# Kernel optimization log

Hardware: AMD Instinct MI355X
Metric: run time of the kernel (lower is better)

## Reference

```python
import jax, jax.numpy as jnp
import numpy as np

EPS_LOG = 1e-10
DECAY = 0.99
RESET_THRESHOLD = 2


def setup_inputs() -> dict:
    key = jax.random.key(0)
    ks = jax.random.split(key, 8)
    B, C_in, T = 4, 1024, 2048
    K, D = 8192, 256
    N = B * T
    return {
        "z": jax.random.normal(ks[0], (B, C_in, T), dtype=jnp.float32),
        "u": jax.random.uniform(ks[1], (N, K), dtype=jnp.float32),
        "Wi": jax.random.normal(ks[2], (D, C_in), dtype=jnp.float32) * 0.02,
        "bi": jax.random.normal(ks[3], (D,), dtype=jnp.float32) * 0.02,
        "Wo": jax.random.normal(ks[4], (C_in, D), dtype=jnp.float32) * 0.02,
        "bo": jax.random.normal(ks[5], (C_in,), dtype=jnp.float32) * 0.02,
        "embedding": jax.random.normal(ks[6], (K, D), dtype=jnp.float32),
        "cluster_size": jnp.zeros((K,), dtype=jnp.float32),
    }


def reference(z, u, Wi, bi, Wo, bo, embedding, cluster_size):
    B, _, T = z.shape
    K, D = embedding.shape
    N = B * T

    # inproj: Conv1d with kernel_size=1 == pointwise linear over channel dim
    z_e = jnp.einsum('bit,di->bdt', z, Wi) + bi[None, :, None]  # (B, D, T)
    z_d = z_e.transpose(0, 2, 1).reshape(N, D)                   # (b t) d

    # squared-euclidean distances via norm expansion
    dist = ((z_d ** 2).sum(axis=1, keepdims=True)
            - 2.0 * (z_d @ embedding.T)
            + (embedding ** 2).sum(axis=1))                      # (N, K)

    # gumbel noise (training=True), softmax_temp = 1.0
    gumbel = -jnp.log(-jnp.log(u + EPS_LOG) + EPS_LOG)
    logits = -dist + gumbel
    y_soft = jax.nn.softmax(logits, axis=-1)                     # (N, K)

    z_q_flat = y_soft @ embedding                                # (N, D)

    # kl_div(log(avg+eps), uniform target of shape (N,K), reduction='sum')
    avg_probs = y_soft.mean(axis=0)                              # (K,)
    inv_k = 1.0 / K
    kl_loss = N * jnp.sum(inv_k * (jnp.log(inv_k) - jnp.log(avg_probs + EPS_LOG)))

    indices = jnp.argmax(y_soft, axis=1)                         # (N,) int

    z_q = z_q_flat.reshape(B, T, D).transpose(0, 2, 1)           # (B, D, T)
    vq_loss = jnp.mean((z_e - jax.lax.stop_gradient(z_q)) ** 2)

    # outproj: Conv1d kernel_size=1
    out = jnp.einsum('bdt,od->bot', z_q, Wo) + bo[None, :, None]  # (B, C_in, T)

    # box_result: active_num uses cluster_size BEFORE the EMA update
    active_num = (cluster_size > RESET_THRESHOLD).sum().astype(z.dtype)
    counts = jnp.zeros((K,), z.dtype).at[indices].add(1.0)       # one-hot column sums
    probs = counts / N                                           # == mean(one_hot, axis=0)
    perplexity = jnp.exp(-jnp.sum(probs * jnp.log(probs + EPS_LOG)))
    new_cluster_size = cluster_size * DECAY + counts * (1.0 - DECAY)

    return out, vq_loss, kl_loss, perplexity, active_num, new_cluster_size
```

## Files before the change

### kernel.cpp

```cpp
#include <hip/hip_runtime.h>
#include <hip/hip_fp16.h>


#define NROWS 8192
#define KCL   8192
#define DDIM  256
#define CIN   1024
#define TSEQ  2048
#define EPSL  1e-10f
#define MHAT  (-140.0f)

#define OUT_SC   (4*CIN*TSEQ)

#define ZD_OFF   0
#define ZQ_OFF   (NROWS*DDIM)
#define E2_OFF   (2*NROWS*DDIM)
#define CS_OFF   (E2_OFF + KCL)
#define CNT_OFF  (CS_OFF + KCL)
#define VQ_OFF   (CNT_OFF + KCL)
#define LINV_OFF (VQ_OFF + 4)

#define ZD2W   0
#define ZQ2W   2097152
#define EBW    4194304
#define ETW    5242880
#define WOBW   6291456
#define ZFW    6422528
#define E2W    7471104
#define C2W    7479296
#define LINVW  7487488
#define CSUMW  7495680
#define CNTW   7503872
#define VQW    7512064
#define PW     7512128
#define ENDW   (PW + 33554432)

using short8v = __attribute__((ext_vector_type(8))) short;
using short4v = __attribute__((ext_vector_type(4))) short;
using f32x16  = __attribute__((ext_vector_type(16))) float;

__device__ __forceinline__ ushort f2bf(float f) {
  unsigned int x = __float_as_uint(f);
  return (ushort)((x + 0x7FFFu + ((x >> 16) & 1u)) >> 16);
}
__device__ __forceinline__ float bf2f(ushort h) {
  return __uint_as_float(((unsigned int)h) << 16);
}
__device__ __forceinline__ short8v pack8(float4 a, float4 b) {
  short8v v;
  v[0] = (short)f2bf(a.x); v[1] = (short)f2bf(a.y);
  v[2] = (short)f2bf(a.z); v[3] = (short)f2bf(a.w);
  v[4] = (short)f2bf(b.x); v[5] = (short)f2bf(b.y);
  v[6] = (short)f2bf(b.z); v[7] = (short)f2bf(b.w);
  return v;
}
__device__ __forceinline__ void gload16(const void* g, void* l) {
  __builtin_amdgcn_global_load_lds(
      (const __attribute__((address_space(1))) unsigned int*)g,
      (__attribute__((address_space(3))) unsigned int*)l, 16, 0, 0);
}


__global__ __launch_bounds__(256) void e2_kernel(const float* __restrict__ E,
                                                 float* __restrict__ e2) {
  const int tid = threadIdx.x;
  const int k = blockIdx.x * 64 + (tid >> 2);
  const int p = tid & 3;
  const float* row = E + (size_t)k * DDIM + p * 64;
  float s = 0.f;
#pragma unroll
  for (int j = 0; j < 16; ++j) {
    const float4 v = *reinterpret_cast<const float4*>(row + j * 4);
    s += v.x * v.x + v.y * v.y + v.z * v.z + v.w * v.w;
  }
  s += __shfl_xor(s, 1);
  s += __shfl_xor(s, 2);
  if (p == 0) e2[k] = s;
}

__global__ __launch_bounds__(256) void e2c2_kernel(const float* __restrict__ E,
                                                   float* __restrict__ e2,
                                                   float* __restrict__ c2) {
  const int tid = threadIdx.x;
  const int k = blockIdx.x * 64 + (tid >> 2);
  const int p = tid & 3;
  const float* row = E + (size_t)k * DDIM + p * 64;
  float s = 0.f;
#pragma unroll
  for (int j = 0; j < 16; ++j) {
    const float4 v = *reinterpret_cast<const float4*>(row + j * 4);
    s += v.x * v.x + v.y * v.y + v.z * v.z + v.w * v.w;
  }
  s += __shfl_xor(s, 1);
  s += __shfl_xor(s, 2);
  if (p == 0) { e2[k] = s; c2[k] = -s - MHAT; }
}

__global__ __launch_bounds__(256) void cvtwob_kernel(const float* __restrict__ W,
                                                     ushort* __restrict__ Wb) {
  const size_t i = ((size_t)blockIdx.x * 256 + threadIdx.x) * 8;
  const float4 a = *reinterpret_cast<const float4*>(W + i);
  const float4 b = *reinterpret_cast<const float4*>(W + i + 4);
  *reinterpret_cast<short8v*>(Wb + i) = pack8(a, b);
}

__global__ __launch_bounds__(256) void etprep_kernel(const float* __restrict__ E,
                                                     ushort* __restrict__ ET,
                                                     ushort* __restrict__ EB) {
  __shared__ float tb[64 * 68];
  const int t = threadIdx.x;
  const int kb = (blockIdx.x & 127) * 64;
  const int db = (blockIdx.x >> 7) * 64;
#pragma unroll
  for (int it = 0; it < 4; ++it) {
    const int r = (t >> 4) + it * 16;
    const int c = (t & 15) * 4;
    const float4 v = *reinterpret_cast<const float4*>(E + (size_t)(kb + r) * DDIM + db + c);
    tb[r * 68 + c] = v.x; tb[r * 68 + c + 1] = v.y;
    tb[r * 68 + c + 2] = v.z; tb[r * 68 + c + 3] = v.w;
    short4v o;
    o[0] = (short)f2bf(v.x); o[1] = (short)f2bf(v.y);
    o[2] = (short)f2bf(v.z); o[3] = (short)f2bf(v.w);
    *reinterpret_cast<short4v*>(EB + (size_t)(kb + r) * DDIM + db + c) = o;
  }
  __syncthreads();
  const int dl = t >> 2, kg = (t & 3) * 16;
  short8v o0, o1;
#pragma unroll
  for (int j = 0; j < 8; ++j) o0[j] = (short)f2bf(tb[(kg + j) * 68 + dl]);
#pragma unroll
  for (int j = 0; j < 8; ++j) o1[j] = (short)f2bf(tb[(kg + 8 + j) * 68 + dl]);
  ushort* dst = ET + (size_t)(db + dl) * KCL + kb + kg;
  *reinterpret_cast<short8v*>(dst) = o0;
  *reinterpret_cast<short8v*>(dst + 8) = o1;
}

__global__ __launch_bounds__(256) void cvtzf_kernel(const float* __restrict__ zd,
                                                    ushort* __restrict__ zf) {
  const int t = threadIdx.x;
  const int g = blockIdx.x;
  const int lane = t & 63, row = lane & 31, half = lane >> 5;
  const float* zr = zd + (size_t)(g * 32 + row) * DDIM + half * 8;
  ushort* dst = zf + ((size_t)g * 16 * 64 + lane) * 8;
#pragma unroll
  for (int i = 0; i < 4; ++i) {
    const int ks = (t >> 6) * 4 + i;
    const float4 a = *reinterpret_cast<const float4*>(zr + ks * 16);
    const float4 b = *reinterpret_cast<const float4*>(zr + ks * 16 + 4);
    *reinterpret_cast<short8v*>(dst + (size_t)ks * 64 * 8) = pack8(a, b);
  }
}

__global__ __launch_bounds__(256) void inproj32_kernel(const float* __restrict__ z,
                                                       const float* __restrict__ Wi,
                                                       const float* __restrict__ bi,
                                                       float* __restrict__ zd) {
  __shared__ float wi_s[32 * 260];
  __shared__ float zc[32 * 32];
  const int tid = threadIdx.x;
  const int nb = blockIdx.x >> 1, cih = blockIdx.x & 1;
  const int n0 = nb * 32;
  const int b = n0 / TSEQ;
  const int t0 = n0 % TSEQ;
  const float* zb = z + (size_t)b * CIN * TSEQ;
  const int ibase = cih * 512;

  const int dg = tid & 63;
  const int d0 = dg * 4;
  const int wv = tid >> 6;
  const int r0 = wv * 8;

  float acc[4][8];
#pragma unroll
  for (int c = 0; c < 4; ++c)
#pragma unroll
    for (int r = 0; r < 8; ++r) acc[c][r] = 0.f;

  for (int i0 = ibase; i0 < ibase + 512; i0 += 32) {
    __syncthreads();
    {
      const int iiq = (tid & 7) * 4;
      const int dt = tid >> 3;
#pragma unroll
      for (int p = 0; p < 8; ++p) {
        const int d = dt + p * 32;
        const float4 w = *reinterpret_cast<const float4*>(Wi + (size_t)d * CIN + i0 + iiq);
        wi_s[(iiq + 0) * 260 + d] = w.x;
        wi_s[(iiq + 1) * 260 + d] = w.y;
        wi_s[(iiq + 2) * 260 + d] = w.z;
        wi_s[(iiq + 3) * 260 + d] = w.w;
      }
      const int rr = tid & 31;
      const int iib = tid >> 5;
#pragma unroll
      for (int p = 0; p < 4; ++p) {
        const int ii = iib + p * 8;
        zc[ii * 32 + rr] = zb[(size_t)(i0 + ii) * TSEQ + t0 + rr];
      }
    }
    __syncthreads();
#pragma unroll
    for (int ii = 0; ii < 32; ++ii) {
      const float4 w = *reinterpret_cast<const float4*>(&wi_s[ii * 260 + d0]);
#pragma unroll
      for (int rq = 0; rq < 2; ++rq) {
        const float4 zv = *reinterpret_cast<const float4*>(&zc[ii * 32 + r0 + rq * 4]);
        const float zz[4] = {zv.x, zv.y, zv.z, zv.w};
#pragma unroll
        for (int q = 0; q < 4; ++q) {
          acc[0][rq * 4 + q] += w.x * zz[q];
          acc[1][rq * 4 + q] += w.y * zz[q];
          acc[2][rq * 4 + q] += w.z * zz[q];
          acc[3][rq * 4 + q] += w.w * zz[q];
        }
      }
    }
  }
  const float4 bv = *reinterpret_cast<const float4*>(bi + d0);
  const float bx = cih ? 0.f : bv.x, by = cih ? 0.f : bv.y;
  const float bz = cih ? 0.f : bv.z, bw = cih ? 0.f : bv.w;
#pragma unroll
  for (int r = 0; r < 8; ++r) {
    float* zr = zd + (size_t)(n0 + r0 + r) * DDIM + d0;
    atomicAdd(zr + 0, acc[0][r] + bx);
    atomicAdd(zr + 1, acc[1][r] + by);
    atomicAdd(zr + 2, acc[2][r] + bz);
    atomicAdd(zr + 3, acc[3][r] + bw);
  }
}

#define FSTEP(KT, CUR, UC, UN)                                                 \
  {                                                                            \
    const int k0 = kbase + (KT) * 32;                                          \
    __syncthreads();            \
    if ((KT) < 15) {                                                           \
      _Pragma("unroll")                                                        \
      for (int pp = 0; pp < 2; ++pp) {                                         \
        const int q = tid + pp * 512, r = q >> 5, c = q & 31;                  \
        gload16(Eb + (size_t)(k0 + 32 + r) * 256 + (size_t)(c ^ (r & 7)) * 8,  \
                &Es[(1 - (CUR)) * 8192 + q * 8]);                              \
      }                                                                        \
      const float* ubn = ubase + k0 + 32 + r31;                                \
      _Pragma("unroll")                                                        \
      for (int reg = 0; reg < 16; ++reg) {                                     \
        const int dr = (reg & 3) + 8 * (reg >> 2);                             \
        UN[reg] = ubn[(size_t)dr << 13];                                       \
      }                                                                        \
    }                                                                          \
    const float ce = c2[k0 + r31];                                             \
    const ushort* Ecur = Es + (CUR) * 8192;                                    \
    f32x16 acc;                                                                \
    _Pragma("unroll")                                                          \
    for (int i = 0; i < 16; ++i) acc[i] = 0.f;                                 \
    _Pragma("unroll")                                                          \
    for (int ks = 0; ks < 16; ++ks) {                                          \
      const int cc = (ks * 2 + half) ^ (r31 & 7);                              \
      const short8v B =                                                        \
          *reinterpret_cast<const short8v*>(Ecur + r31 * 256 + cc * 8);        \
      acc = __builtin_amdgcn_mfma_f32_32x32x16_bf16(A[ks], B, acc, 0, 0, 0);   \
    }                                                                          \
    ushort* pdst = P + (size_t)rowu * KCL + k0 + r31;                          \
    _Pragma("unroll")                                                          \
    for (int reg = 0; reg < 16; ++reg) {                                       \
      const int dr = (reg & 3) + 8 * (reg >> 2);                               \
      const float D = 1e-10f - __logf(UC[reg] + 1e-10f);                       \
      const float pe = __fdividef(__expf(fmaf(acc[reg], 2.f, ce)), D);         \
      pdst[(size_t)dr << 13] = f2bf(pe);                                       \
    }                                                                          \
  }

__global__ __launch_bounds__(512, 2) void flash4_kernel(
    const ushort* __restrict__ ZF, const float* __restrict__ u,
    const ushort* __restrict__ Eb, const float* __restrict__ c2,
    ushort* __restrict__ P) {
  __shared__ ushort Es[2 * 32 * 256];
  const int tid = threadIdx.x;
  const int l = tid & 63, w = tid >> 6;
  const int half = l >> 5;
  const int swz = (blockIdx.x & 7) * 64 + (blockIdx.x >> 3);
  const int nb = swz & 31, kq = swz >> 5;
  const int n0 = nb * 256;
  const int kbase = kq * 512;
  const int r31 = l & 31;

  short8v A[16];
  {
    const ushort* zf = ZF + ((size_t)(nb * 8 + w) * 16 * 64 + l) * 8;
#pragma unroll
    for (int ks = 0; ks < 16; ++ks)
      A[ks] = *reinterpret_cast<const short8v*>(zf + (size_t)ks * 512);
  }

  const int rowu = n0 + w * 32 + 4 * half;
  const float* ubase = u + ((size_t)rowu << 13);

#pragma unroll
  for (int pp = 0; pp < 2; ++pp) {
    const int q = tid + pp * 512, r = q >> 5, c = q & 31;
    gload16(Eb + (size_t)(kbase + r) * 256 + (size_t)(c ^ (r & 7)) * 8, &Es[q * 8]);
  }
  float uA[16], uB[16];
  {
    const float* ub = ubase + kbase + r31;
#pragma unroll
    for (int reg = 0; reg < 16; ++reg) {
      const int dr = (reg & 3) + 8 * (reg >> 2);
      uA[reg] = ub[(size_t)dr << 13];
    }
  }

  for (int kt2 = 0; kt2 < 16; kt2 += 2) {
    FSTEP(kt2, 0, uA, uB);
    FSTEP(kt2 + 1, 1, uB, uA);
  }
}

__global__ __launch_bounds__(256) void rowpass_kernel(
    const ushort* __restrict__ P, const float* __restrict__ zd,
    const float* __restrict__ E, const float* __restrict__ e2,
    const float* __restrict__ u, float* __restrict__ linv,
    float* __restrict__ counts) {
  const int l = threadIdx.x & 63;
  const int w = threadIdx.x >> 6;
  const int n = blockIdx.x * 4 + w;
  const ushort* pr = P + (size_t)n * KCL;
  float lsum = 0.f;
  float bv[4] = {-1.f, -1.f, -1.f, -1.f};
  int bi[4] = {0x7fffffff, 0x7fffffff, 0x7fffffff, 0x7fffffff};
  for (int it = 0; it < 16; ++it) {
    const short8v v = *reinterpret_cast<const short8v*>(pr + it * 512 + l * 8);
#pragma unroll
    for (int j = 0; j < 8; ++j) {
      const float f = bf2f((ushort)v[j]);
      lsum += f;
      const int kk = it * 512 + l * 8 + j;
      const bool c0 = f > bv[0], c1 = f > bv[1];
      const float n1 = c0 ? bv[0] : f; const int i1 = c0 ? bi[0] : kk;
      bv[1] = c1 ? n1 : bv[1]; bi[1] = c1 ? i1 : bi[1];
      bv[0] = c0 ? f : bv[0];  bi[0] = c0 ? kk : bi[0];
    }
  }
#pragma unroll
  for (int mk = 1; mk < 64; mk <<= 1) {
    lsum += __shfl_xor(lsum, mk);
    float ov[4]; int oi[4];
#pragma unroll
    for (int i = 0; i < 4; ++i) { ov[i] = __shfl_xor(bv[i], mk); oi[i] = __shfl_xor(bi[i], mk); }
#pragma unroll
    for (int i = 0; i < 4; ++i) {
      const float f = ov[i]; const int kk = oi[i];
      const bool c0 = (f > bv[0]) || (f == bv[0] && kk < bi[0]);
      const bool c1 = (f > bv[1]) || (f == bv[1] && kk < bi[1]);
      const bool c2 = (f > bv[2]) || (f == bv[2] && kk < bi[2]);
      const bool c3 = (f > bv[3]) || (f == bv[3] && kk < bi[3]);
      const float n3 = c2 ? bv[2] : f; const int i3 = c2 ? bi[2] : kk;
      const float n2 = c1 ? bv[1] : f; const int i2 = c1 ? bi[1] : kk;
      const float n1 = c0 ? bv[0] : f; const int i1 = c0 ? bi[0] : kk;
      bv[3] = c3 ? n3 : bv[3]; bi[3] = c3 ? i3 : bi[3];
      bv[2] = c2 ? n2 : bv[2]; bi[2] = c2 ? i2 : bi[2];
      bv[1] = c1 ? n1 : bv[1]; bi[1] = c1 ? i1 : bi[1];
      bv[0] = c0 ? f : bv[0];  bi[0] = c0 ? kk : bi[0];
    }
  }
  const float4 zv = *reinterpret_cast<const float4*>(zd + (size_t)n * DDIM + l * 4);
  float best = -1e30f; int besti = 0x7fffffff;
#pragma unroll
  for (int c = 0; c < 4; ++c) {
    const int kc = bi[c];
    const float4 ev = *reinterpret_cast<const float4*>(E + (size_t)kc * DDIM + l * 4);
    float d = zv.x * ev.x + zv.y * ev.y + zv.z * ev.z + zv.w * ev.w;
#pragma unroll
    for (int mk = 1; mk < 64; mk <<= 1) d += __shfl_xor(d, mk);
    const float uu = u[(size_t)n * KCL + kc];
    const float D = 1e-10f - __logf(uu + 1e-10f);
    const float g = -__logf(D);
    const float lg = 2.f * d - e2[kc] + g;
    if (lg > best || (lg == best && kc < besti)) { best = lg; besti = kc; }
  }
  if (l == 0) {
    atomicAdd(&counts[besti], 1.f);
    linv[n] = 1.f / lsum;
  }
}

__global__ __launch_bounds__(512, 2) void pv2_kernel(
    const ushort* __restrict__ P, const ushort* __restrict__ ET,
    const float* __restrict__ linv, float* __restrict__ parts,
    float* __restrict__ colsum) {
  __shared__ ushort ps[64 * 64];
  __shared__ ushort es[256 * 64];
  __shared__ float linv_s[64];
  const int tid = threadIdx.x;
  const int l = tid & 63, w = tid >> 6;
  const int half = l >> 5;
  const int r31 = l & 31;
  const int swz = (blockIdx.x & 7) * 64 + (blockIdx.x >> 3);
  const int nb = swz & 127, ks = swz >> 7;
  const int n0 = nb * 64;
  const int kc0 = ks * 2048;
  const int nw = w & 1, dw = w >> 1;

  if (tid < 64) linv_s[tid] = linv[n0 + tid];

  f32x16 acc0, acc1;
#pragma unroll
  for (int i = 0; i < 16; ++i) { acc0[i] = 0.f; acc1[i] = 0.f; }

  short8v rp, re[4];
  {
    const int r = tid >> 3, c = tid & 7;
    rp = *reinterpret_cast<const short8v*>(P + (size_t)(n0 + r) * KCL + kc0 + c * 8);
#pragma unroll
    for (int pp = 0; pp < 4; ++pp) {
      const int q = tid * 4 + pp; const int rr = q >> 3, cc = q & 7;
      re[pp] = *reinterpret_cast<const short8v*>(ET + (size_t)rr * KCL + kc0 + cc * 8);
    }
  }
  for (int t = 0; t < 32; ++t) {
    {
      const int r = tid >> 3, c = tid & 7;
      *reinterpret_cast<short8v*>(ps + r * 64 + ((c ^ (r & 7))) * 8) = rp;
    }
#pragma unroll
    for (int pp = 0; pp < 4; ++pp) {
      const int q = tid * 4 + pp; const int rr = q >> 3, cc = q & 7;
      *reinterpret_cast<short8v*>(es + rr * 64 + ((cc ^ (rr & 7))) * 8) = re[pp];
    }
    __syncthreads();
    if (t < 31) {
      const int kc = kc0 + (t + 1) * 64;
      {
        const int r = tid >> 3, c = tid & 7;
        rp = *reinterpret_cast<const short8v*>(P + (size_t)(n0 + r) * KCL + kc + c * 8);
      }
#pragma unroll
      for (int pp = 0; pp < 4; ++pp) {
        const int q = tid * 4 + pp; const int rr = q >> 3, cc = q & 7;
        re[pp] = *reinterpret_cast<const short8v*>(ET + (size_t)rr * KCL + kc + cc * 8);
      }
    }
#pragma unroll
    for (int ksn = 0; ksn < 4; ++ksn) {
      const int cc = ksn * 2 + half;
      short8v a, b0, b1;
      { const int r = nw * 32 + r31;      a  = *reinterpret_cast<const short8v*>(ps + r * 64 + ((cc ^ (r & 7))) * 8); }
      { const int r = dw * 64 + r31;      b0 = *reinterpret_cast<const short8v*>(es + r * 64 + ((cc ^ (r & 7))) * 8); }
      { const int r = dw * 64 + 32 + r31; b1 = *reinterpret_cast<const short8v*>(es + r * 64 + ((cc ^ (r & 7))) * 8); }
      acc0 = __builtin_amdgcn_mfma_f32_32x32x16_bf16(a, b0, acc0, 0, 0, 0);
      acc1 = __builtin_amdgcn_mfma_f32_32x32x16_bf16(a, b1, acc1, 0, 0, 0);
    }
    {
      const int c = tid >> 3;
      const int rb = tid & 7;
      float csp = 0.f;
#pragma unroll
      for (int r8 = 0; r8 < 8; ++r8) {
        const int r = rb + r8 * 8;
        const int chunk = (c >> 3) ^ (r & 7);
        csp += bf2f(ps[r * 64 + chunk * 8 + (c & 7)]) * linv_s[r];
      }
      csp += __shfl_xor(csp, 1);
      csp += __shfl_xor(csp, 2);
      csp += __shfl_xor(csp, 4);
      if (rb == 0) atomicAdd(&colsum[kc0 + t * 64 + c], csp);
    }
    __syncthreads();
  }
  float* pbase = parts + (size_t)ks * NROWS * DDIM;
#pragma unroll
  for (int reg = 0; reg < 16; ++reg) {
    const int dr = (reg & 3) + 8 * (reg >> 2) + 4 * half;
    float* zr = pbase + (size_t)(n0 + nw * 32 + dr) * DDIM + dw * 64 + r31;
    zr[0]  = acc0[reg];
    zr[32] = acc1[reg];
  }
}

__global__ __launch_bounds__(256) void zqred_kernel(const float* __restrict__ parts,
                                                    const float* __restrict__ linv,
                                                    const float* __restrict__ zd,
                                                    float* __restrict__ zq,
                                                    float* __restrict__ vqs) {
  const size_t i = ((size_t)blockIdx.x * 256 + threadIdx.x) * 8;
  const int n = (int)(i >> 8);
  const float lv = linv[n];
  float s = 0.f;
#pragma unroll
  for (int j = 0; j < 8; j += 4) {
    float4 p0 = *reinterpret_cast<const float4*>(parts + i + j);
    const float4 p1 = *reinterpret_cast<const float4*>(parts + i + j + (size_t)NROWS * DDIM);
    const float4 p2 = *reinterpret_cast<const float4*>(parts + i + j + (size_t)2 * NROWS * DDIM);
    const float4 p3 = *reinterpret_cast<const float4*>(parts + i + j + (size_t)3 * NROWS * DDIM);
    const float4 a = *reinterpret_cast<const float4*>(zd + i + j);
    float4 o;
    o.x = (p0.x + p1.x + p2.x + p3.x) * lv;
    o.y = (p0.y + p1.y + p2.y + p3.y) * lv;
    o.z = (p0.z + p1.z + p2.z + p3.z) * lv;
    o.w = (p0.w + p1.w + p2.w + p3.w) * lv;
    *reinterpret_cast<float4*>(zq + i + j) = o;
    const float dx = a.x - o.x, dy = a.y - o.y, dz = a.z - o.z, dw = a.w - o.w;
    s += dx * dx + dy * dy + dz * dz + dw * dw;
  }
#pragma unroll
  for (int mk = 1; mk < 64; mk <<= 1) s += __shfl_xor(s, mk);
  if ((threadIdx.x & 63) == 0) atomicAdd(vqs, s);
}

__global__ __launch_bounds__(256) void outproj2_kernel(const float* __restrict__ zq,
                                                       const ushort* __restrict__ Wob,
                                                       const float* __restrict__ bo,
                                                       float* __restrict__ outp) {
  extern __shared__ char smem[];
  ushort* zs = (ushort*)smem;
  ushort* wsld = zs + 64 * 256;
  const int tid = threadIdx.x;
  const int l = tid & 63, w = tid >> 6;
  const int half = l >> 5;
  const int nb = blockIdx.x >> 4, ob = blockIdx.x & 15;
  const int n0 = nb * 64, o0 = ob * 64;
  const int nw = w & 1, ow = w >> 1;
  {
    const int row = tid >> 2, seg = tid & 3;
    const float* zr = zq + (size_t)(n0 + row) * DDIM + seg * 64;
    const ushort* wr = Wob + (size_t)(o0 + row) * DDIM + seg * 64;
#pragma unroll
    for (int g = 0; g < 8; ++g) {
      const float4 a = *reinterpret_cast<const float4*>(zr + g * 8);
      const float4 b = *reinterpret_cast<const float4*>(zr + g * 8 + 4);
      const int c = seg * 8 + g;
      *reinterpret_cast<short8v*>(zs + row * 256 + ((c ^ (row & 7))) * 8) = pack8(a, b);
      const short8v wv = *reinterpret_cast<const short8v*>(wr + g * 8);
      *reinterpret_cast<short8v*>(wsld + row * 256 + ((c ^ (row & 7))) * 8) = wv;
    }
  }
  __syncthreads();
  f32x16 acc;
#pragma unroll
  for (int i = 0; i < 16; ++i) acc[i] = 0.f;
#pragma unroll
  for (int ksn = 0; ksn < 16; ++ksn) {
    const int cc = ksn * 2 + half;
    const int ra = nw * 32 + (l & 31);
    const int rb = ow * 32 + (l & 31);
    const short8v a = *reinterpret_cast<const short8v*>(zs + ra * 256 + ((cc ^ (ra & 7))) * 8);
    const short8v b = *reinterpret_cast<const short8v*>(wsld + rb * 256 + ((cc ^ (rb & 7))) * 8);
    acc = __builtin_amdgcn_mfma_f32_32x32x16_bf16(a, b, acc, 0, 0, 0);
  }
  const int o = o0 + ow * 32 + (l & 31);
  const float bvv = bo[o];
  const int nbase = n0 + nw * 32 + 4 * half;
#pragma unroll
  for (int rq = 0; rq < 4; ++rq) {
    const int n = nbase + rq * 8;
    const int b = n >> 11;
    const int tt = n & 2047;
    float4 ov;
    ov.x = acc[rq * 4 + 0] + bvv;
    ov.y = acc[rq * 4 + 1] + bvv;
    ov.z = acc[rq * 4 + 2] + bvv;
    ov.w = acc[rq * 4 + 3] + bvv;
    *reinterpret_cast<float4*>(outp + ((size_t)b * CIN + o) * TSEQ + tt) = ov;
  }
}

template <bool STORE_LG>
__global__ __launch_bounds__(512) void flash_kernel(
    const float* __restrict__ zd, const float* __restrict__ u,
    const float* __restrict__ E, const float* __restrict__ e2g,
    float* __restrict__ zq, float* __restrict__ colsum,
    float* __restrict__ counts, float* __restrict__ vqsum,
    float* __restrict__ linvg, __half* __restrict__ lgbuf) {
  extern __shared__ float lds[];
  float* zs = lds;
  float* es = zs + 32 * 260;
  float* e2t = es + 64 * 260;
  float* cst = e2t + 64;
  float* red = cst + 64;

  const int tid = threadIdx.x;
  const int lane = tid & 63;
  const int wv = tid >> 6;
  const int r = (lane >> 4) & 3;
  const int kg = lane & 15;
  const int row = wv * 4 + r;
  const int n0 = blockIdx.x * 32;
  const int n = n0 + row;

  {
    const int rr = tid >> 4;
    const int iq = tid & 15;
#pragma unroll
    for (int p = 0; p < 4; ++p) {
      const int i = iq * 16 + p * 4;
      *reinterpret_cast<float4*>(&zs[rr * 260 + i]) =
          *reinterpret_cast<const float4*>(zd + (size_t)(n0 + rr) * DDIM + i);
    }
  }

  float4 accp[4];
#pragma unroll
  for (int s = 0; s < 4; ++s) accp[s] = make_float4(0.f, 0.f, 0.f, 0.f);
  float lsum = 0.f;
  float best = -1e30f;
  int bidx = 0;

  const float* zrow = zs + row * 260;

  for (int t = 0; t < KCL / 64; ++t) {
    const int k0 = t * 64;
    __syncthreads();
    {
      const int iq = tid & 15;
#pragma unroll
      for (int pp = 0; pp < 2; ++pp) {
        const int kk = (tid >> 4) + pp * 32;
#pragma unroll
        for (int p = 0; p < 4; ++p) {
          const int i = iq * 16 + p * 4;
          *reinterpret_cast<float4*>(&es[kk * 260 + i]) =
              *reinterpret_cast<const float4*>(E + (size_t)(k0 + kk) * DDIM + i);
        }
      }
      if (tid < 64) e2t[tid] = e2g[k0 + tid];
    }
    __syncthreads();

    float acc4[4] = {0.f, 0.f, 0.f, 0.f};
#pragma unroll 4
    for (int i = 0; i < DDIM; i += 4) {
      const float4 zv = *reinterpret_cast<const float4*>(zrow + i);
#pragma unroll
      for (int jj = 0; jj < 4; ++jj) {
        const float4 ev = *reinterpret_cast<const float4*>(&es[(kg + jj * 16) * 260 + i]);
        acc4[jj] += zv.x * ev.x + zv.y * ev.y + zv.z * ev.z + zv.w * ev.w;
      }
    }

    float p4[4];
    float tmax = -1e30f;
    int tidx = 0;
#pragma unroll
    for (int jj = 0; jj < 4; ++jj) {
      const int kk = kg + jj * 16;
      const float uu = u[(size_t)n * KCL + k0 + kk];
      const float g = -__logf(-__logf(uu + EPSL) + EPSL);
      const float lt = 2.f * acc4[jj] - e2t[kk] + g - MHAT;
      const float pe = __expf(lt);
      p4[jj] = pe;
      lsum += pe;
      if (lt > tmax) { tmax = lt; tidx = k0 + kk; }
    }
#pragma unroll
    for (int mk = 1; mk <= 8; mk <<= 1) {
      const float ov = __shfl_xor(tmax, mk);
      const int oi = __shfl_xor(tidx, mk);
      if (ov > tmax || (ov == tmax && oi < tidx)) { tmax = ov; tidx = oi; }
    }
    if (tmax > best) { best = tmax; bidx = tidx; }

#pragma unroll
    for (int jj = 0; jj < 4; ++jj) {
#pragma unroll 4
      for (int q = 0; q < 16; ++q) {
        const int kk = jj * 16 + q;
        const float yv = __shfl(p4[jj], (lane & 48) | q);
        const float* erow = &es[kk * 260 + kg * 16];
#pragma unroll
        for (int s = 0; s < 4; ++s) {
          const int c = (s + kg) & 3;
          const float4 ev = *reinterpret_cast<const float4*>(erow + c * 4);
          accp[s].x += yv * ev.x;
          accp[s].y += yv * ev.y;
          accp[s].z += yv * ev.z;
          accp[s].w += yv * ev.w;
        }
      }
    }
  }

#pragma unroll
  for (int mk = 1; mk <= 8; mk <<= 1) lsum += __shfl_xor(lsum, mk);
  const float linv = 1.0f / lsum;

  if (kg == 0) {
    atomicAdd(&counts[bidx], 1.0f);
    linvg[n] = linv;
  }

  float vqp = 0.f;
#pragma unroll
  for (int s = 0; s < 4; ++s) {
    const int c = (s + kg) & 3;
    const int d = kg * 16 + c * 4;
    float4 o;
    o.x = accp[s].x * linv;
    o.y = accp[s].y * linv;
    o.z = accp[s].z * linv;
    o.w = accp[s].w * linv;
    *reinterpret_cast<float4*>(zq + (size_t)n * DDIM + d) = o;
    const float4 zv = *reinterpret_cast<const float4*>(zrow + d);
    const float dx = zv.x - o.x, dy = zv.y - o.y, dz = zv.z - o.z, dw = zv.w - o.w;
    vqp += dx * dx + dy * dy + dz * dz + dw * dw;
  }
#pragma unroll
  for (int mk = 1; mk <= 32; mk <<= 1) vqp += __shfl_xor(vqp, mk);
  if (lane == 0) red[wv] = vqp;
  __syncthreads();
  if (tid == 0) {
    float s = 0.f;
#pragma unroll
    for (int ww = 0; ww < 8; ++ww) s += red[ww];
    atomicAdd(vqsum, s);
  }

  if (!STORE_LG) {
    if (tid < 64) cst[tid] = 0.f;
    for (int t = 0; t < KCL / 64; ++t) {
      const int k0 = t * 64;
      __syncthreads();
      {
        const int iq = tid & 15;
#pragma unroll
        for (int pp = 0; pp < 2; ++pp) {
          const int kk = (tid >> 4) + pp * 32;
#pragma unroll
          for (int p = 0; p < 4; ++p) {
            const int i = iq * 16 + p * 4;
            *reinterpret_cast<float4*>(&es[kk * 260 + i]) =
                *reinterpret_cast<const float4*>(E + (size_t)(k0 + kk) * DDIM + i);
          }
        }
        if (tid < 64) e2t[tid] = e2g[k0 + tid];
      }
      __syncthreads();
      float acc4[4] = {0.f, 0.f, 0.f, 0.f};
#pragma unroll 4
      for (int i = 0; i < DDIM; i += 4) {
        const float4 zv = *reinterpret_cast<const float4*>(zrow + i);
#pragma unroll
        for (int jj = 0; jj < 4; ++jj) {
          const float4 ev = *reinterpret_cast<const float4*>(&es[(kg + jj * 16) * 260 + i]);
          acc4[jj] += zv.x * ev.x + zv.y * ev.y + zv.z * ev.z + zv.w * ev.w;
        }
      }
      float cs4[4];
#pragma unroll
      for (int jj = 0; jj < 4; ++jj) {
        const int kk = kg + jj * 16;
        const float uu = u[(size_t)n * KCL + k0 + kk];
        const float g = -__logf(-__logf(uu + EPSL) + EPSL);
        const float lt = 2.f * acc4[jj] - e2t[kk] + g - MHAT;
        cs4[jj] = __expf(lt) * linv;
      }
#pragma unroll
      for (int mk = 16; mk <= 32; mk <<= 1)
#pragma unroll
        for (int jj = 0; jj < 4; ++jj) cs4[jj] += __shfl_xor(cs4[jj], mk);
      if (lane < 16) {
#pragma unroll
        for (int jj = 0; jj < 4; ++jj) atomicAdd(&cst[kg + jj * 16], cs4[jj]);
      }
      __syncthreads();
      if (tid < 64) {
        atomicAdd(&colsum[k0 + tid], cst[tid]);
        cst[tid] = 0.f;
      }
    }
  }
}

__global__ __launch_bounds__(256) void outproj_kernel(const float* __restrict__ zq,
                                                      const float* __restrict__ Wo,
                                                      const float* __restrict__ bo,
                                                      float* __restrict__ outp) {
  __shared__ float wo_s[32 * 260];
  __shared__ float zc[32 * 68];
  const int tid = threadIdx.x;
  const int n0 = (blockIdx.x >> 2) * 64;
  const int ot = (blockIdx.x & 3) * 256;
  const int b = n0 / TSEQ;
  const int t0 = n0 % TSEQ;

  const int og = tid & 63;
  const int o0 = og * 4;
  const int wv = tid >> 6;
  const int r0 = wv * 16;

  float acc[4][16];
#pragma unroll
  for (int c = 0; c < 4; ++c)
#pragma unroll
    for (int r = 0; r < 16; ++r) acc[c][r] = 0.f;

  for (int dd = 0; dd < DDIM; dd += 32) {
    __syncthreads();
    {
      const int ccq = (tid & 7) * 4;
      const int oq = tid >> 3;
#pragma unroll
      for (int p = 0; p < 8; ++p) {
        const int oo = oq + p * 32;
        const float4 w = *reinterpret_cast<const float4*>(Wo + (size_t)(ot + oo) * DDIM + dd + ccq);
        wo_s[(ccq + 0) * 260 + oo] = w.x;
        wo_s[(ccq + 1) * 260 + oo] = w.y;
        wo_s[(ccq + 2) * 260 + oo] = w.z;
        wo_s[(ccq + 3) * 260 + oo] = w.w;
      }
#pragma unroll
      for (int p = 0; p < 2; ++p) {
        const int rr = oq + p * 32;
        const float4 v = *reinterpret_cast<const float4*>(zq + (size_t)(n0 + rr) * DDIM + dd + ccq);
        zc[(ccq + 0) * 68 + rr] = v.x;
        zc[(ccq + 1) * 68 + rr] = v.y;
        zc[(ccq + 2) * 68 + rr] = v.z;
        zc[(ccq + 3) * 68 + rr] = v.w;
      }
    }
    __syncthreads();
#pragma unroll
    for (int cc = 0; cc < 32; ++cc) {
      const float4 w = *reinterpret_cast<const float4*>(&wo_s[cc * 260 + o0]);
#pragma unroll
      for (int rq = 0; rq < 4; ++rq) {
        const float4 zv = *reinterpret_cast<const float4*>(&zc[cc * 68 + r0 + rq * 4]);
        const float zz[4] = {zv.x, zv.y, zv.z, zv.w};
#pragma unroll
        for (int q = 0; q < 4; ++q) {
          acc[0][rq * 4 + q] += w.x * zz[q];
          acc[1][rq * 4 + q] += w.y * zz[q];
          acc[2][rq * 4 + q] += w.z * zz[q];
          acc[3][rq * 4 + q] += w.w * zz[q];
        }
      }
    }
  }
  const float4 bv = *reinterpret_cast<const float4*>(bo + ot + o0);
  float* ob = outp + (size_t)b * CIN * TSEQ + t0;
  const float bb[4] = {bv.x, bv.y, bv.z, bv.w};
#pragma unroll
  for (int c = 0; c < 4; ++c) {
#pragma unroll
    for (int rq = 0; rq < 4; ++rq) {
      float4 o;
      o.x = acc[c][rq * 4 + 0] + bb[c];
      o.y = acc[c][rq * 4 + 1] + bb[c];
      o.z = acc[c][rq * 4 + 2] + bb[c];
      o.w = acc[c][rq * 4 + 3] + bb[c];
      *reinterpret_cast<float4*>(ob + (size_t)(ot + o0 + c) * TSEQ + r0 + rq * 4) = o;
    }
  }
}

__global__ __launch_bounds__(256) void finalize_kernel(
    const float* __restrict__ colsum, const float* __restrict__ counts,
    const float* __restrict__ vqsum, const float* __restrict__ csin,
    float* __restrict__ outsc, float* __restrict__ ncs) {
  __shared__ float rS[3][4];
  const int tid = threadIdx.x;
  const int lane = tid & 63;
  const int wv = tid >> 6;
  float sLog = 0.f, sH = 0.f, sAct = 0.f;
  for (int k = tid; k < KCL; k += 256) {
    const float avg = colsum[k] * (1.0f / NROWS);
    sLog += __logf(avg + EPSL);
    const float pb = counts[k] * (1.0f / NROWS);
    sH += pb * __logf(pb + EPSL);
    sAct += (csin[k] > 2.0f) ? 1.f : 0.f;
    ncs[k] = csin[k] * 0.99f + counts[k] * 0.01f;
  }
#pragma unroll
  for (int mk = 1; mk <= 32; mk <<= 1) {
    sLog += __shfl_xor(sLog, mk);
    sH += __shfl_xor(sH, mk);
    sAct += __shfl_xor(sAct, mk);
  }
  if (lane == 0) { rS[0][wv] = sLog; rS[1][wv] = sH; rS[2][wv] = sAct; }
  __syncthreads();
  if (tid == 0) {
    float SL = 0.f, SH = 0.f, SA = 0.f;
#pragma unroll
    for (int w = 0; w < 4; ++w) { SL += rS[0][w]; SH += rS[1][w]; SA += rS[2][w]; }
    outsc[0] = vqsum[0] * (1.0f / ((float)NROWS * (float)DDIM));
    outsc[1] = (float)NROWS * __logf(1.0f / (float)KCL) - SL;
    outsc[2] = __expf(-SH);
    outsc[3] = SA;
  }
}

extern "C" void kernel_launch(void* const* d_in, const int* in_sizes, int n_in,
                              void* d_out, int out_size, void* d_ws, size_t ws_size,
                              hipStream_t stream) {
  (void)in_sizes; (void)n_in; (void)out_size;
  const float* z = (const float*)d_in[0];
  const float* u = (const float*)d_in[1];
  const float* Wi = (const float*)d_in[2];
  const float* bi = (const float*)d_in[3];
  const float* Wo = (const float*)d_in[4];
  const float* bo = (const float*)d_in[5];
  const float* E = (const float*)d_in[6];
  const float* csin = (const float*)d_in[7];
  float* outp = (float*)d_out;
  float* ws = (float*)d_ws;

  const size_t needNew = (size_t)ENDW * 4;
  if (ws_size >= needNew) {
    ushort* EB = (ushort*)(ws + EBW);
    ushort* ET = (ushort*)(ws + ETW);
    ushort* WOB = (ushort*)(ws + WOBW);
    ushort* ZF = (ushort*)(ws + ZFW);
    ushort* P = (ushort*)(ws + PW);

    hipMemsetAsync((void*)(ws + CSUMW), 0, (size_t)(2 * KCL + 64) * 4, stream);
    hipMemsetAsync((void*)(ws + ZD2W), 0, (size_t)NROWS * DDIM * 4, stream);

    e2c2_kernel<<<KCL / 64, 256, 0, stream>>>(E, ws + E2W, ws + C2W);
    etprep_kernel<<<512, 256, 0, stream>>>(E, ET, EB);
    cvtwob_kernel<<<128, 256, 0, stream>>>(Wo, WOB);
    inproj32_kernel<<<512, 256, 0, stream>>>(z, Wi, bi, ws + ZD2W);
    cvtzf_kernel<<<NROWS / 32, 256, 0, stream>>>(ws + ZD2W, ZF);

    flash4_kernel<<<512, 512, 0, stream>>>(ZF, u, EB, ws + C2W, P);
    rowpass_kernel<<<NROWS / 4, 256, 0, stream>>>(P, ws + ZD2W, E, ws + E2W, u,
                                                  ws + LINVW, ws + CNTW);
    pv2_kernel<<<512, 512, 0, stream>>>(P, ET, ws + LINVW, outp, ws + CSUMW);
    zqred_kernel<<<1024, 256, 0, stream>>>(outp, ws + LINVW, ws + ZD2W,
                                           ws + ZQ2W, ws + VQW);

    hipFuncSetAttribute(reinterpret_cast<const void*>(&outproj2_kernel),
                        hipFuncAttributeMaxDynamicSharedMemorySize, 65536);
    outproj2_kernel<<<2048, 256, 65536, stream>>>(ws + ZQ2W, WOB, bo, outp);
    finalize_kernel<<<1, 256, 0, stream>>>(ws + CSUMW, ws + CNTW, ws + VQW,
                                           csin, outp + OUT_SC, outp + OUT_SC + 4);
  } else {
    hipMemsetAsync((void*)(ws + CS_OFF), 0, (size_t)(2 * KCL + 1) * sizeof(float), stream);
    hipMemsetAsync((void*)(ws + ZD_OFF), 0, (size_t)NROWS * DDIM * 4, stream);
    e2_kernel<<<KCL / 64, 256, 0, stream>>>(E, ws + E2_OFF);
    inproj32_kernel<<<512, 256, 0, stream>>>(z, Wi, bi, ws + ZD_OFF);
    const int ldsB = (32 * 260 + 64 * 260 + 64 + 64 + 16) * 4;
    hipFuncSetAttribute(reinterpret_cast<const void*>(&flash_kernel<false>),
                        hipFuncAttributeMaxDynamicSharedMemorySize, ldsB);
    flash_kernel<false><<<NROWS / 32, 512, ldsB, stream>>>(
        ws + ZD_OFF, u, E, ws + E2_OFF, ws + ZQ_OFF, ws + CS_OFF, ws + CNT_OFF,
        ws + VQ_OFF, ws + LINV_OFF, (__half*)nullptr);
    outproj_kernel<<<(NROWS / 64) * 4, 256, 0, stream>>>(ws + ZQ_OFF, Wo, bo, outp);
    finalize_kernel<<<1, 256, 0, stream>>>(ws + CS_OFF, ws + CNT_OFF, ws + VQ_OFF,
                                           csin, outp + OUT_SC, outp + OUT_SC + 4);
  }
}
```

Before: 512.0 us.

## Fuse row sums and top-2 argmax into flash kernel, drop P re-read pass

```diff
diff --git a/kernel.cpp b/kernel.cpp
--- a/kernel.cpp
+++ b/kernel.cpp
@@ -25,7 +25,7 @@
 #define EBW    4194304
 #define ETW    5242880
 #define WOBW   6291456
-#define ZFW    6422528
+#define ZDBW   6422528
 #define E2W    7471104
 #define C2W    7479296
 #define LINVW  7487488
@@ -34,6 +34,9 @@
 #define VQW    7512064
 #define PW     7512128
 #define ENDW   (PW + 33554432)
+#define LSPW   ZQ2W
+#define CVW    (ZQ2W + 131072)
+#define CIW    (ZQ2W + 393216)
 
 using short8v = __attribute__((ext_vector_type(8))) short;
 using short4v = __attribute__((ext_vector_type(4))) short;
@@ -133,22 +136,6 @@
   ushort* dst = ET + (size_t)(db + dl) * KCL + kb + kg;
   *reinterpret_cast<short8v*>(dst) = o0;
   *reinterpret_cast<short8v*>(dst + 8) = o1;
-}
-
-__global__ __launch_bounds__(256) void cvtzf_kernel(const float* __restrict__ zd,
-                                                    ushort* __restrict__ zf) {
-  const int t = threadIdx.x;
-  const int g = blockIdx.x;
-  const int lane = t & 63, row = lane & 31, half = lane >> 5;
-  const float* zr = zd + (size_t)(g * 32 + row) * DDIM + half * 8;
-  ushort* dst = zf + ((size_t)g * 16 * 64 + lane) * 8;
-#pragma unroll
-  for (int i = 0; i < 4; ++i) {
-    const int ks = (t >> 6) * 4 + i;
-    const float4 a = *reinterpret_cast<const float4*>(zr + ks * 16);
-    const float4 b = *reinterpret_cast<const float4*>(zr + ks * 16 + 4);
-    *reinterpret_cast<short8v*>(dst + (size_t)ks * 64 * 8) = pack8(a, b);
-  }
 }
 
 __global__ __launch_bounds__(256) void inproj32_kernel(const float* __restrict__ z,
@@ -229,7 +216,7 @@
   }
 }
 
-#define FSTEP(KT, CUR, UC, UN)                                                 \
+#define FSS(KT, CUR, UC, UN)                                                   \
   {                                                                            \
     const int k0 = kbase + (KT) * 32;                                          \
     __syncthreads();            \
@@ -240,14 +227,11 @@
         gload16(Eb + (size_t)(k0 + 32 + r) * 256 + (size_t)(c ^ (r & 7)) * 8,  \
                 &Es[(1 - (CUR)) * 8192 + q * 8]);                              \
       }                                                                        \
-      const float* ubn = ubase + k0 + 32 + r31;                                \
+      const float* ubn = ubase + k0 + 32 + 4 * half;                           \
       _Pragma("unroll")                                                        \
-      for (int reg = 0; reg < 16; ++reg) {                                     \
-        const int dr = (reg & 3) + 8 * (reg >> 2);                             \
-        UN[reg] = ubn[(size_t)dr << 13];                                       \
-      }                                                                        \
+      for (int q = 0; q < 4; ++q)                                              \
+        UN[q] = *reinterpret_cast<const float4*>(ubn + q * 8);                 \
     }                                                                          \
-    const float ce = c2[k0 + r31];                                             \
     const ushort* Ecur = Es + (CUR) * 8192;                                    \
     f32x16 acc;                                                                \
     _Pragma("unroll")                                                          \
@@ -255,25 +239,40 @@
     _Pragma("unroll")                                                          \
     for (int ks = 0; ks < 16; ++ks) {                                          \
       const int cc = (ks * 2 + half) ^ (r31 & 7);                              \
-      const short8v B =                                                        \
+      const short8v Af =                                                       \
           *reinterpret_cast<const short8v*>(Ecur + r31 * 256 + cc * 8);        \
-      acc = __builtin_amdgcn_mfma_f32_32x32x16_bf16(A[ks], B, acc, 0, 0, 0);   \
+      acc = __builtin_amdgcn_mfma_f32_32x32x16_bf16(Af, ZB[ks], acc, 0, 0, 0); \
     }                                                                          \
-    ushort* pdst = P + (size_t)rowu * KCL + k0 + r31;                          \
+    ushort* pdst = P + (size_t)n * KCL + k0 + 4 * half;                        \
     _Pragma("unroll")                                                          \
-    for (int reg = 0; reg < 16; ++reg) {                                       \
-      const int dr = (reg & 3) + 8 * (reg >> 2);                               \
-      const float D = 1e-10f - __logf(UC[reg] + 1e-10f);                       \
-      const float pe = __fdividef(__expf(fmaf(acc[reg], 2.f, ce)), D);         \
-      pdst[(size_t)dr << 13] = f2bf(pe);                                       \
+    for (int q = 0; q < 4; ++q) {                                              \
+      const float uu[4] = {UC[q].x, UC[q].y, UC[q].z, UC[q].w};                \
+      short4v st;                                                              \
+      _Pragma("unroll")                                                        \
+      for (int j = 0; j < 4; ++j) {                                            \
+        const int reg = q * 4 + j;                                             \
+        const int kcl = k0 + q * 8 + 4 * half + j;                             \
+        const float ce = c2s[kcl - kbase];                                     \
+        const float D = 1e-10f - __logf(uu[j] + 1e-10f);                       \
+        const float pe = __fdividef(__expf(fmaf(acc[reg], 2.f, ce)), D);       \
+        psum += pe;                                                            \
+        const bool cA = pe > b0v, cB = pe > b1v;                               \
+        const float nv = cA ? b0v : pe; const int ni = cA ? b0i : kcl;         \
+        b1v = cB ? nv : b1v; b1i = cB ? ni : b1i;                              \
+        b0v = cA ? pe : b0v; b0i = cA ? kcl : b0i;                             \
+        st[j] = (short)f2bf(pe);                                               \
+      }                                                                        \
+      *reinterpret_cast<short4v*>(pdst + q * 8) = st;                          \
     }                                                                          \
   }
 
-__global__ __launch_bounds__(512, 2) void flash4_kernel(
-    const ushort* __restrict__ ZF, const float* __restrict__ u,
+__global__ __launch_bounds__(512, 2) void flashS_kernel(
+    const ushort* __restrict__ ZDB, const float* __restrict__ u,
     const ushort* __restrict__ Eb, const float* __restrict__ c2,
-    ushort* __restrict__ P) {
+    ushort* __restrict__ P, float* __restrict__ lsp,
+    float* __restrict__ candv, int* __restrict__ candi) {
   __shared__ ushort Es[2 * 32 * 256];
+  __shared__ float c2s[512];
   const int tid = threadIdx.x;
   const int l = tid & 63, w = tid >> 6;
   const int half = l >> 5;
@@ -282,67 +281,84 @@
   const int n0 = nb * 256;
   const int kbase = kq * 512;
   const int r31 = l & 31;
-
-  short8v A[16];
+  const int n = n0 + w * 32 + r31;
+
+  short8v ZB[16];
   {
-    const ushort* zf = ZF + ((size_t)(nb * 8 + w) * 16 * 64 + l) * 8;
+    const ushort* zr = ZDB + (size_t)n * DDIM + half * 8;
 #pragma unroll
     for (int ks = 0; ks < 16; ++ks)
-      A[ks] = *reinterpret_cast<const short8v*>(zf + (size_t)ks * 512);
-  }
-
-  const int rowu = n0 + w * 32 + 4 * half;
-  const float* ubase = u + ((size_t)rowu << 13);
+      ZB[ks] = *reinterpret_cast<const short8v*>(zr + ks * 16);
+  }
+
+  const float* ubase = u + ((size_t)n << 13);
+  c2s[tid] = c2[kbase + tid];
 
 #pragma unroll
   for (int pp = 0; pp < 2; ++pp) {
     const int q = tid + pp * 512, r = q >> 5, c = q & 31;
     gload16(Eb + (size_t)(kbase + r) * 256 + (size_t)(c ^ (r & 7)) * 8, &Es[q * 8]);
   }
-  float uA[16], uB[16];
+  float4 uA[4], uB[4];
   {
-    const float* ub = ubase + kbase + r31;
-#pragma unroll
-    for (int reg = 0; reg < 16; ++reg) {
-      const int dr = (reg & 3) + 8 * (reg >> 2);
-      uA[reg] = ub[(size_t)dr << 13];
-    }
-  }
+    const float* ub = ubase + kbase + 4 * half;
+#pragma unroll
+    for (int q = 0; q < 4; ++q)
+      uA[q] = *reinterpret_cast<const float4*>(ub + q * 8);
+  }
+
+  float psum = 0.f;
+  float b0v = -1.f, b1v = -1.f;
+  int b0i = 0x7fffffff, b1i = 0x7fffffff;
 
   for (int kt2 = 0; kt2 < 16; kt2 += 2) {
-    FSTEP(kt2, 0, uA, uB);
-    FSTEP(kt2 + 1, 1, uB, uA);
-  }
-}
-
-__global__ __launch_bounds__(256) void rowpass_kernel(
-    const ushort* __restrict__ P, const float* __restrict__ zd,
+    FSS(kt2, 0, uA, uB);
+    FSS(kt2 + 1, 1, uB, uA);
+  }
+
+  psum += __shfl_xor(psum, 32);
+  {
+    const float ov0 = __shfl_xor(b0v, 32); const int oi0 = __shfl_xor(b0i, 32);
+    const float ov1 = __shfl_xor(b1v, 32); const int oi1 = __shfl_xor(b1i, 32);
+    {
+      const bool cA = (ov0 > b0v) || (ov0 == b0v && oi0 < b0i);
+      const bool cB = (ov0 > b1v) || (ov0 == b1v && oi0 < b1i);
+      const float nv = cA ? b0v : ov0; const int ni = cA ? b0i : oi0;
+      b1v = cB ? nv : b1v; b1i = cB ? ni : b1i;
+      b0v = cA ? ov0 : b0v; b0i = cA ? oi0 : b0i;
+    }
+    {
+      const bool cA = (ov1 > b0v) || (ov1 == b0v && oi1 < b0i);
+      const bool cB = (ov1 > b1v) || (ov1 == b1v && oi1 < b1i);
+      const float nv = cA ? b0v : ov1; const int ni = cA ? b0i : oi1;
+      b1v = cB ? nv : b1v; b1i = cB ? ni : b1i;
+      b0v = cA ? ov1 : b0v; b0i = cA ? oi1 : b0i;
+    }
+  }
+  if (half == 0) {
+    lsp[kq * NROWS + n] = psum;
+    candv[(kq * 2 + 0) * NROWS + n] = b0v;
+    candi[(kq * 2 + 0) * NROWS + n] = b0i;
+    candv[(kq * 2 + 1) * NROWS + n] = b1v;
+    candi[(kq * 2 + 1) * NROWS + n] = b1i;
+  }
+}
+
+__global__ __launch_bounds__(256) void rowfin_kernel(
+    const float* __restrict__ lsp, const float* __restrict__ candv,
+    const int* __restrict__ candi, const float* __restrict__ zd,
     const float* __restrict__ E, const float* __restrict__ e2,
     const float* __restrict__ u, float* __restrict__ linv,
     float* __restrict__ counts) {
   const int l = threadIdx.x & 63;
   const int w = threadIdx.x >> 6;
   const int n = blockIdx.x * 4 + w;
-  const ushort* pr = P + (size_t)n * KCL;
-  float lsum = 0.f;
+
   float bv[4] = {-1.f, -1.f, -1.f, -1.f};
   int bi[4] = {0x7fffffff, 0x7fffffff, 0x7fffffff, 0x7fffffff};
-  for (int it = 0; it < 16; ++it) {
-    const short8v v = *reinterpret_cast<const short8v*>(pr + it * 512 + l * 8);
-#pragma unroll
-    for (int j = 0; j < 8; ++j) {
-      const float f = bf2f((ushort)v[j]);
-      lsum += f;
-      const int kk = it * 512 + l * 8 + j;
-      const bool c0 = f > bv[0], c1 = f > bv[1];
-      const float n1 = c0 ? bv[0] : f; const int i1 = c0 ? bi[0] : kk;
-      bv[1] = c1 ? n1 : bv[1]; bi[1] = c1 ? i1 : bi[1];
-      bv[0] = c0 ? f : bv[0];  bi[0] = c0 ? kk : bi[0];
-    }
-  }
+  if (l < 32) { bv[0] = candv[l * NROWS + n]; bi[0] = candi[l * NROWS + n]; }
 #pragma unroll
   for (int mk = 1; mk < 64; mk <<= 1) {
-    lsum += __shfl_xor(lsum, mk);
     float ov[4]; int oi[4];
 #pragma unroll
     for (int i = 0; i < 4; ++i) { ov[i] = __shfl_xor(bv[i], mk); oi[i] = __shfl_xor(bi[i], mk); }
@@ -362,6 +378,9 @@
       bv[0] = c0 ? f : bv[0];  bi[0] = c0 ? kk : bi[0];
     }
   }
+  float ls = (l < 16) ? lsp[l * NROWS + n] : 0.f;
+#pragma unroll
+  for (int mk = 1; mk <= 8; mk <<= 1) ls += __shfl_xor(ls, mk);
   const float4 zv = *reinterpret_cast<const float4*>(zd + (size_t)n * DDIM + l * 4);
   float best = -1e30f; int besti = 0x7fffffff;
 #pragma unroll
@@ -379,16 +398,15 @@
   }
   if (l == 0) {
     atomicAdd(&counts[besti], 1.f);
-    linv[n] = 1.f / lsum;
-  }
-}
-
-__global__ __launch_bounds__(512, 2) void pv2_kernel(
+    linv[n] = 1.f / ls;
+  }
+}
+
+__global__ __launch_bounds__(512, 2) void pvS_kernel(
     const ushort* __restrict__ P, const ushort* __restrict__ ET,
     const float* __restrict__ linv, float* __restrict__ parts,
     float* __restrict__ colsum) {
-  __shared__ ushort ps[64 * 64];
-  __shared__ ushort es[256 * 64];
+  __shared__ ushort ps[2][64 * 64];
   __shared__ float linv_s[64];
   const int tid = threadIdx.x;
   const int l = tid & 63, w = tid >> 6;
@@ -399,6 +417,7 @@
   const int n0 = nb * 64;
   const int kc0 = ks * 2048;
   const int nw = w & 1, dw = w >> 1;
+  const int sr = tid >> 3, sc = tid & 7;
 
   if (tid < 64) linv_s[tid] = linv[n0 + tid];
 
@@ -406,46 +425,30 @@
 #pragma unroll
   for (int i = 0; i < 16; ++i) { acc0[i] = 0.f; acc1[i] = 0.f; }
 
-  short8v rp, re[4];
-  {
-    const int r = tid >> 3, c = tid & 7;
-    rp = *reinterpret_cast<const short8v*>(P + (size_t)(n0 + r) * KCL + kc0 + c * 8);
-#pragma unroll
-    for (int pp = 0; pp < 4; ++pp) {
-      const int q = tid * 4 + pp; const int rr = q >> 3, cc = q & 7;
-      re[pp] = *reinterpret_cast<const short8v*>(ET + (size_t)rr * KCL + kc0 + cc * 8);
-    }
-  }
+  gload16(P + (size_t)(n0 + sr) * KCL + kc0 + (size_t)(sc ^ (sr & 7)) * 8,
+          &ps[0][tid * 8]);
+
   for (int t = 0; t < 32; ++t) {
-    {
-      const int r = tid >> 3, c = tid & 7;
-      *reinterpret_cast<short8v*>(ps + r * 64 + ((c ^ (r & 7))) * 8) = rp;
-    }
-#pragma unroll
-    for (int pp = 0; pp < 4; ++pp) {
-      const int q = tid * 4 + pp; const int rr = q >> 3, cc = q & 7;
-      *reinterpret_cast<short8v*>(es + rr * 64 + ((cc ^ (rr & 7))) * 8) = re[pp];
-    }
+    const int cur = t & 1;
+    const int kc = kc0 + t * 64;
     __syncthreads();
     if (t < 31) {
-      const int kc = kc0 + (t + 1) * 64;
-      {
-        const int r = tid >> 3, c = tid & 7;
-        rp = *reinterpret_cast<const short8v*>(P + (size_t)(n0 + r) * KCL + kc + c * 8);
-      }
-#pragma unroll
-      for (int pp = 0; pp < 4; ++pp) {
-        const int q = tid * 4 + pp; const int rr = q >> 3, cc = q & 7;
-        re[pp] = *reinterpret_cast<const short8v*>(ET + (size_t)rr * KCL + kc + cc * 8);
-      }
+      gload16(P + (size_t)(n0 + sr) * KCL + kc + 64 + (size_t)(sc ^ (sr & 7)) * 8,
+              &ps[1 - cur][tid * 8]);
     }
 #pragma unroll
     for (int ksn = 0; ksn < 4; ++ksn) {
       const int cc = ksn * 2 + half;
       short8v a, b0, b1;
-      { const int r = nw * 32 + r31;      a  = *reinterpret_cast<const short8v*>(ps + r * 64 + ((cc ^ (r & 7))) * 8); }
-      { const int r = dw * 64 + r31;      b0 = *reinterpret_cast<const short8v*>(es + r * 64 + ((cc ^ (r & 7))) * 8); }
-      { const int r = dw * 64 + 32 + r31; b1 = *reinterpret_cast<const short8v*>(es + r * 64 + ((cc ^ (r & 7))) * 8); }
+      {
+        const int r = nw * 32 + r31;
+        a = *reinterpret_cast<const short8v*>(&ps[cur][r * 64 + ((cc ^ (r & 7))) * 8]);
+      }
+      {
+        const ushort* etb = ET + (size_t)(dw * 64 + r31) * KCL + kc + cc * 8;
+        b0 = *reinterpret_cast<const short8v*>(etb);
+        b1 = *reinterpret_cast<const short8v*>(etb + (size_t)32 * KCL);
+      }
       acc0 = __builtin_amdgcn_mfma_f32_32x32x16_bf16(a, b0, acc0, 0, 0, 0);
       acc1 = __builtin_amdgcn_mfma_f32_32x32x16_bf16(a, b1, acc1, 0, 0, 0);
     }
@@ -457,14 +460,13 @@
       for (int r8 = 0; r8 < 8; ++r8) {
         const int r = rb + r8 * 8;
         const int chunk = (c >> 3) ^ (r & 7);
-        csp += bf2f(ps[r * 64 + chunk * 8 + (c & 7)]) * linv_s[r];
+        csp += bf2f(ps[cur][r * 64 + chunk * 8 + (c & 7)]) * linv_s[r];
       }
       csp += __shfl_xor(csp, 1);
       csp += __shfl_xor(csp, 2);
       csp += __shfl_xor(csp, 4);
-      if (rb == 0) atomicAdd(&colsum[kc0 + t * 64 + c], csp);
-    }
-    __syncthreads();
+      if (rb == 0) atomicAdd(&colsum[kc + c], csp);
+    }
   }
   float* pbase = parts + (size_t)ks * NROWS * DDIM;
 #pragma unroll
@@ -907,7 +909,7 @@
     ushort* EB = (ushort*)(ws + EBW);
     ushort* ET = (ushort*)(ws + ETW);
     ushort* WOB = (ushort*)(ws + WOBW);
-    ushort* ZF = (ushort*)(ws + ZFW);
+    ushort* ZDB = (ushort*)(ws + ZDBW);
     ushort* P = (ushort*)(ws + PW);
 
     hipMemsetAsync((void*)(ws + CSUMW), 0, (size_t)(2 * KCL + 64) * 4, stream);
@@ -917,12 +919,15 @@
     etprep_kernel<<<512, 256, 0, stream>>>(E, ET, EB);
     cvtwob_kernel<<<128, 256, 0, stream>>>(Wo, WOB);
     inproj32_kernel<<<512, 256, 0, stream>>>(z, Wi, bi, ws + ZD2W);
-    cvtzf_kernel<<<NROWS / 32, 256, 0, stream>>>(ws + ZD2W, ZF);
-
-    flash4_kernel<<<512, 512, 0, stream>>>(ZF, u, EB, ws + C2W, P);
-    rowpass_kernel<<<NROWS / 4, 256, 0, stream>>>(P, ws + ZD2W, E, ws + E2W, u,
-                                                  ws + LINVW, ws + CNTW);
-    pv2_kernel<<<512, 512, 0, stream>>>(P, ET, ws + LINVW, outp, ws + CSUMW);
+    cvtwob_kernel<<<1024, 256, 0, stream>>>(ws + ZD2W, ZDB);
+
+    flashS_kernel<<<512, 512, 0, stream>>>(ZDB, u, EB, ws + C2W, P,
+                                           ws + LSPW, ws + CVW, (int*)(ws + CIW));
+    rowfin_kernel<<<NROWS / 4, 256, 0, stream>>>(ws + LSPW, ws + CVW,
+                                                 (const int*)(ws + CIW),
+                                                 ws + ZD2W, E, ws + E2W, u,
+                                                 ws + LINVW, ws + CNTW);
+    pvS_kernel<<<512, 512, 0, stream>>>(P, ET, ws + LINVW, outp, ws + CSUMW);
     zqred_kernel<<<1024, 256, 0, stream>>>(outp, ws + LINVW, ws + ZD2W,
                                            ws + ZQ2W, ws + VQW);
 
```

Result: slower. 606.9 us, median of 3 (+18.5%).
